# Kernel tuning notes

Hardware: AMD Instinct MI355X
Metric: run time of the kernel (lower is better)

Reference implementation:

```python
import jax, jax.numpy as jnp
import numpy as np

N_NODES = 100000


def _sage_conv(x, src, dst, w_l, b_l, w_r):
    # PyG SAGEConv (aggr='mean', root_weight=True):
    #   out = lin_l(mean_{j in N(i)} x_j) + lin_r(x_i)
    # messages flow src (row 0) -> dst (row 1)
    msgs = x[src]                                             # [E, d]
    agg = jax.ops.segment_sum(msgs, dst, num_segments=N_NODES)  # [N, d]
    cnt = jax.ops.segment_sum(jnp.ones((src.shape[0], 1), x.dtype), dst,
                              num_segments=N_NODES)           # [N, 1]
    mean = agg / jnp.maximum(cnt, 1.0)
    return mean @ w_l + b_l + x @ w_r


def setup_inputs() -> dict:
    key = jax.random.key(0)
    ks = jax.random.split(key, 8)
    in_dim, hid, out = 128, 64, 128
    n_edges = 1600000
    x = jax.random.normal(ks[0], (N_NODES, in_dim), dtype=jnp.float32)
    edge_index = jax.random.randint(ks[1], (2, n_edges), 0, N_NODES, dtype=jnp.int64)
    s1 = 1.0 / np.sqrt(in_dim)
    s2 = 1.0 / np.sqrt(hid)
    return {
        "x": x,
        "edge_index": edge_index,
        "w1_l": jax.random.uniform(ks[2], (in_dim, hid), jnp.float32, -s1, s1),
        "b1": jnp.zeros((hid,), jnp.float32),
        "w1_r": jax.random.uniform(ks[3], (in_dim, hid), jnp.float32, -s1, s1),
        "w2_l": jax.random.uniform(ks[4], (hid, out), jnp.float32, -s2, s2),
        "b2": jnp.zeros((out,), jnp.float32),
        "w2_r": jax.random.uniform(ks[5], (hid, out), jnp.float32, -s2, s2),
    }


def reference(x, edge_index, w1_l, b1, w1_r, w2_l, b2, w2_r):
    src, dst = edge_index[0], edge_index[1]
    h = jax.nn.relu(_sage_conv(x, src, dst, w1_l, b1, w1_r))
    h = _sage_conv(h, src, dst, w2_l, b2, w2_r)
    return h
```

## Files before the change

### kernel.cpp

```cpp
#include <hip/hip_runtime.h>

#define N_NODES 100000
#define NBUCK   782
#define P1TILE  8192
#define MAXB    4096

typedef __bf16 bf16x8 __attribute__((ext_vector_type(8)));
typedef float floatx4 __attribute__((ext_vector_type(4)));
typedef float floatx2 __attribute__((ext_vector_type(2)));

static __device__ __forceinline__ unsigned short f2bf(float f) {
  unsigned u = __float_as_uint(f);
  u += 0x7fff + ((u >> 16) & 1);
  return (unsigned short)(u >> 16);
}

__global__ __launch_bounds__(256) void bucket_count_kernel(
    const int* __restrict__ dst, int* __restrict__ bucket_cnt, int n_edges) {
  __shared__ int hist[NBUCK];
  for (int b = threadIdx.x; b < NBUCK; b += 256) hist[b] = 0;
  __syncthreads();
  int stride = gridDim.x * 256;
  for (int e = blockIdx.x * 256 + threadIdx.x; e < n_edges; e += stride)
    atomicAdd(&hist[dst[e] >> 7], 1);
  __syncthreads();
  for (int b = threadIdx.x; b < NBUCK; b += 256) {
    int c = hist[b];
    if (c) atomicAdd(&bucket_cnt[b], c);
  }
}

__global__ __launch_bounds__(256) void bucket_scan_kernel(
    const int* __restrict__ bucket_cnt, int* __restrict__ bucket_base,
    int* __restrict__ bucket_cursor) {
  __shared__ int tmp[256];
  int t = threadIdx.x;
  int loc[4];
  int s = 0;
  #pragma unroll
  for (int j = 0; j < 4; ++j) {
    int idx = 4 * t + j;
    loc[j] = s;
    s += (idx < NBUCK) ? bucket_cnt[idx] : 0;
  }
  tmp[t] = s;
  __syncthreads();
  for (int off = 1; off < 256; off <<= 1) {
    int u = (t >= off) ? tmp[t - off] : 0;
    __syncthreads();
    tmp[t] += u;
    __syncthreads();
  }
  int excl = tmp[t] - s;
  #pragma unroll
  for (int j = 0; j < 4; ++j) {
    int idx = 4 * t + j;
    if (idx < NBUCK) {
      int v = excl + loc[j];
      bucket_base[idx] = v;
      bucket_cursor[idx] = v;
    }
  }
  if (t == 255) bucket_base[NBUCK] = tmp[255];
}

__global__ __launch_bounds__(256) void bucket_partition_kernel(
    const int* __restrict__ src, const int* __restrict__ dst,
    int* __restrict__ bucket_cursor, unsigned* __restrict__ pairs,
    int n_edges) {
  __shared__ int hist[NBUCK];
  __shared__ int scan_[NBUCK];
  __shared__ int gbase[NBUCK];
  __shared__ int tmp[256];
  __shared__ int2 sorted[P1TILE];
  int t = threadIdx.x;
  long e0 = (long)blockIdx.x * P1TILE;
  int n = (int)min((long)P1TILE, (long)n_edges - e0);

  for (int b = t; b < NBUCK; b += 256) hist[b] = 0;
  __syncthreads();
  for (int i = t; i < n; i += 256) atomicAdd(&hist[dst[e0 + i] >> 7], 1);
  __syncthreads();

  int loc[4];
  int s = 0;
  #pragma unroll
  for (int j = 0; j < 4; ++j) {
    int idx = 4 * t + j;
    loc[j] = s;
    s += (idx < NBUCK) ? hist[idx] : 0;
  }
  tmp[t] = s;
  __syncthreads();
  for (int off = 1; off < 256; off <<= 1) {
    int u = (t >= off) ? tmp[t - off] : 0;
    __syncthreads();
    tmp[t] += u;
    __syncthreads();
  }
  int excl = tmp[t] - s;
  #pragma unroll
  for (int j = 0; j < 4; ++j) {
    int idx = 4 * t + j;
    if (idx < NBUCK) scan_[idx] = excl + loc[j];
  }
  __syncthreads();

  for (int b = t; b < NBUCK; b += 256) {
    int c = hist[b];
    gbase[b] = c ? atomicAdd(&bucket_cursor[b], c) : 0;
    hist[b] = scan_[b];
  }
  __syncthreads();

  for (int i = t; i < n; i += 256) {
    int sv = src[e0 + i];
    int dv = dst[e0 + i];
    int r = atomicAdd(&hist[dv >> 7], 1);
    sorted[r] = make_int2(sv, dv);
  }
  __syncthreads();

  for (int i = t; i < n; i += 256) {
    int2 p = sorted[i];
    int b = p.y >> 7;
    unsigned pk = (unsigned)p.x | ((unsigned)(p.y & 127) << 17);
    pairs[gbase[b] + (i - scan_[b])] = pk;
  }
}

__global__ __launch_bounds__(256) void bucket_csr_kernel(
    const unsigned* __restrict__ pairs, const int* __restrict__ bucket_base,
    int* __restrict__ offsets, int* __restrict__ src_sorted,
    int n_nodes, int n_edges) {
  __shared__ unsigned sp[MAXB];
  __shared__ int lout[MAXB];
  __shared__ int ndeg[128];
  __shared__ int nsc[128];
  int b = blockIdx.x;
  int node0 = b << 7;
  int t = threadIdx.x;
  int ebeg = bucket_base[b];
  int eend = bucket_base[b + 1];
  int m = eend - ebeg;
  bool fits = (m <= MAXB);
  if (t < 128) ndeg[t] = 0;
  __syncthreads();

  if (fits) {
    for (int i = t; i < m; i += 256) {
      unsigned p = pairs[ebeg + i];
      sp[i] = p;
      atomicAdd(&ndeg[p >> 17], 1);
    }
  } else {
    for (int i = t; i < m; i += 256)
      atomicAdd(&ndeg[pairs[ebeg + i] >> 17], 1);
  }
  __syncthreads();

  if (t < 128) nsc[t] = ndeg[t];
  __syncthreads();
  for (int off = 1; off < 128; off <<= 1) {
    int u = 0;
    if (t < 128 && t >= off) u = nsc[t - off];
    __syncthreads();
    if (t < 128) nsc[t] += u;
    __syncthreads();
  }
  if (t < 128) {
    int excl = nsc[t] - ndeg[t];
    int node = node0 + t;
    if (node < n_nodes) offsets[node] = ebeg + excl;
    ndeg[t] = excl;
  }
  if (b == NBUCK - 1 && t == 0) offsets[n_nodes] = n_edges;
  __syncthreads();

  if (fits) {
    for (int i = t; i < m; i += 256) {
      unsigned p = sp[i];
      int r = atomicAdd(&ndeg[p >> 17], 1);
      lout[r] = (int)(p & 0x1FFFFu);
    }
    __syncthreads();
    for (int i = t; i < m; i += 256) src_sorted[ebeg + i] = lout[i];
  } else {
    for (int i = t; i < m; i += 256) {
      unsigned p = pairs[ebeg + i];
      int r = atomicAdd(&ndeg[p >> 17], 1);
      src_sorted[ebeg + r] = (int)(p & 0x1FFFFu);
    }
  }
}

__global__ __launch_bounds__(128) void prep_weights_kernel(
    const float* __restrict__ w1_l, const float* __restrict__ w1_r,
    const float* __restrict__ w2_l, const float* __restrict__ w2_r,
    unsigned short* __restrict__ Wt1, unsigned short* __restrict__ Wt2) {
  int n = blockIdx.x, k = threadIdx.x;
  float v1 = (n < 64) ? w1_l[k * 64 + n] : w1_r[k * 64 + (n - 64)];
  Wt1[n * 128 + k] = f2bf(v1);
  float v2 = (k < 64) ? w2_l[k * 128 + n] : w2_r[(k - 64) * 128 + n];
  Wt2[n * 128 + k] = f2bf(v2);
}

template <int BIAS_MODE, bool OUT_BF16, bool A_F32>
__global__ __launch_bounds__(256) void mfma_gemm_kernel(
    const void* __restrict__ Av, const unsigned short* __restrict__ Wt,
    const float* __restrict__ bias, void* __restrict__ Y, int M) {
  __shared__ unsigned short As[64 * 136];
  int node0 = blockIdx.x * 64;
  int t = threadIdx.x;
  if (A_F32) {
    const float* A = (const float*)Av;
    #pragma unroll
    for (int i = 0; i < 8; ++i) {
      int c = t + i * 256;
      int row = c >> 5, c4 = (c & 31) * 4;
      float4 v = make_float4(0.f, 0.f, 0.f, 0.f);
      if (node0 + row < M) v = *(const float4*)&A[(long)(node0 + row) * 128 + c4];
      ushort4 o;
      o.x = f2bf(v.x); o.y = f2bf(v.y); o.z = f2bf(v.z); o.w = f2bf(v.w);
      *(ushort4*)&As[row * 136 + c4] = o;
    }
  } else {
    const unsigned short* A = (const unsigned short*)Av;
    #pragma unroll
    for (int i = 0; i < 4; ++i) {
      int c = t + i * 256;
      int row = c >> 4, c8 = (c & 15) * 8;
      uint4 v = make_uint4(0u, 0u, 0u, 0u);
      if (node0 + row < M) v = *(const uint4*)&A[(long)(node0 + row) * 128 + c8];
      *(uint4*)&As[row * 136 + c8] = v;
    }
  }
  __syncthreads();
  int w = t >> 6, lane = t & 63;
  int m = lane & 15, q = lane >> 4;
  int col0 = w * 32;
  floatx4 acc[4][2];
  #pragma unroll
  for (int rt = 0; rt < 4; ++rt)
    #pragma unroll
    for (int ct = 0; ct < 2; ++ct) acc[rt][ct] = (floatx4){0.f, 0.f, 0.f, 0.f};

  #pragma unroll
  for (int ks = 0; ks < 4; ++ks) {
    bf16x8 b0 = *(const bf16x8*)&Wt[(col0 + m) * 128 + ks * 32 + q * 8];
    bf16x8 b1 = *(const bf16x8*)&Wt[(col0 + 16 + m) * 128 + ks * 32 + q * 8];
    #pragma unroll
    for (int rt = 0; rt < 4; ++rt) {
      bf16x8 a = *(const bf16x8*)&As[(rt * 16 + m) * 136 + ks * 32 + q * 8];
      acc[rt][0] = __builtin_amdgcn_mfma_f32_16x16x32_bf16(a, b0, acc[rt][0], 0, 0, 0);
      acc[rt][1] = __builtin_amdgcn_mfma_f32_16x16x32_bf16(a, b1, acc[rt][1], 0, 0, 0);
    }
  }
  #pragma unroll
  for (int ct = 0; ct < 2; ++ct) {
    int col = col0 + ct * 16 + m;
    float bv = 0.f;
    if (BIAS_MODE == 1) bv = (col >= 64) ? bias[col - 64] : 0.f;
    if (BIAS_MODE == 2) bv = bias[col];
    #pragma unroll
    for (int rt = 0; rt < 4; ++rt) {
      #pragma unroll
      for (int i = 0; i < 4; ++i) {
        int row = node0 + rt * 16 + q * 4 + i;
        if (row >= M) continue;
        float v = acc[rt][ct][i] + bv;
        if (OUT_BF16) ((unsigned short*)Y)[(long)row * 128 + col] = f2bf(v);
        else          ((float*)Y)[(long)row * 128 + col] = v;
      }
    }
  }
}

#define ACC_V(v)                                                               \
  do {                                                                         \
    a01 += (floatx2){__uint_as_float((v).x << 16),                             \
                     __uint_as_float((v).x & 0xffff0000u)};                    \
    a23 += (floatx2){__uint_as_float((v).y << 16),                             \
                     __uint_as_float((v).y & 0xffff0000u)};                    \
    a45 += (floatx2){__uint_as_float((v).z << 16),                             \
                     __uint_as_float((v).z & 0xffff0000u)};                    \
    a67 += (floatx2){__uint_as_float((v).w << 16),                             \
                     __uint_as_float((v).w & 0xffff0000u)};                    \
  } while (0)

template <bool FUSE_RELU>
__global__ __launch_bounds__(256) void aggregate_bf16_kernel(
    const unsigned short* __restrict__ gsrc, const unsigned short* __restrict__ zadd,
    unsigned short* __restrict__ outp, const int* __restrict__ offsets,
    const int* __restrict__ src_sorted, int n_nodes) {
  int wid = (blockIdx.x * 256 + threadIdx.x) >> 6;
  int lane = threadIdx.x & 63;
  int node8 = wid << 3;
  if (node8 >= n_nodes) return;
  int sub = lane >> 3;
  int sl  = lane & 7;
  int node = node8 + sub;
  bool nvalid = (node < n_nodes);
  int beg = nvalid ? offsets[node] : 0;
  int end = nvalid ? offsets[node + 1] : 0;
  int deg = end - beg;

  int R = deg;
  R = max(R, __shfl_xor(R, 8, 64));
  R = max(R, __shfl_xor(R, 16, 64));
  R = max(R, __shfl_xor(R, 32, 64));

  const unsigned short* base = gsrc + sl * 8;
  floatx2 a01 = {0.f, 0.f}, a23 = {0.f, 0.f}, a45 = {0.f, 0.f}, a67 = {0.f, 0.f};

  int sidx = (sl < deg) ? src_sorted[beg + sl] : 0;
  int srcl = (lane & 56);

  for (int b = 0; b * 8 < R; ++b) {
    int sidx_nxt = 0;
    int nb = (b + 1) * 8;
    if (nb < R) {
      int p = nb + sl;
      if (p < deg) sidx_nxt = src_sorted[beg + p];
    }
    int k0 = b * 8;
    #pragma unroll
    for (int j = 0; j < 8; ++j) {
      int s = __shfl(sidx, srcl | j, 64);
      if (k0 + j < deg) {
        uint4 v = *(const uint4*)(base + (long)s * 128);
        ACC_V(v);
      }
    }
    sidx = sidx_nxt;
  }

  if (nvalid) {
    float inv = 1.f / fmaxf((float)deg, 1.f);
    float r[8];
    r[0] = a01.x * inv; r[1] = a01.y * inv;
    r[2] = a23.x * inv; r[3] = a23.y * inv;
    r[4] = a45.x * inv; r[5] = a45.y * inv;
    r[6] = a67.x * inv; r[7] = a67.y * inv;
    if (FUSE_RELU) {
      uint4 z = *(const uint4*)&zadd[(long)node * 128 + sl * 8];
      r[0] = fmaxf(r[0] + __uint_as_float(z.x << 16), 0.f);
      r[1] = fmaxf(r[1] + __uint_as_float(z.x & 0xffff0000u), 0.f);
      r[2] = fmaxf(r[2] + __uint_as_float(z.y << 16), 0.f);
      r[3] = fmaxf(r[3] + __uint_as_float(z.y & 0xffff0000u), 0.f);
      r[4] = fmaxf(r[4] + __uint_as_float(z.z << 16), 0.f);
      r[5] = fmaxf(r[5] + __uint_as_float(z.z & 0xffff0000u), 0.f);
      r[6] = fmaxf(r[6] + __uint_as_float(z.w << 16), 0.f);
      r[7] = fmaxf(r[7] + __uint_as_float(z.w & 0xffff0000u), 0.f);
    }
    uint4 ov;
    ov.x = (unsigned)f2bf(r[0]) | ((unsigned)f2bf(r[1]) << 16);
    ov.y = (unsigned)f2bf(r[2]) | ((unsigned)f2bf(r[3]) << 16);
    ov.z = (unsigned)f2bf(r[4]) | ((unsigned)f2bf(r[5]) << 16);
    ov.w = (unsigned)f2bf(r[6]) | ((unsigned)f2bf(r[7]) << 16);
    *(uint4*)&outp[(long)node * 128 + sl * 8] = ov;
  }
}
#undef ACC_V

extern "C" void kernel_launch(void* const* d_in, const int* in_sizes, int n_in,
                              void* d_out, int out_size, void* d_ws, size_t ws_size,
                              hipStream_t stream) {
  const float* x    = (const float*)d_in[0];
  const int*   ei   = (const int*)d_in[1];
  const float* w1_l = (const float*)d_in[2];
  const float* b1   = (const float*)d_in[3];
  const float* w1_r = (const float*)d_in[4];
  const float* w2_l = (const float*)d_in[5];
  const float* b2   = (const float*)d_in[6];
  const float* w2_r = (const float*)d_in[7];
  float* out = (float*)d_out;

  const int E = in_sizes[1] / 2;
  const int* src = ei;
  const int* dst = ei + E;

  unsigned short* ZB1 = (unsigned short*)d_ws;
  unsigned short* ZB2 = ZB1 + (long)N_NODES * 128;
  unsigned short* Wt1 = ZB2 + (long)N_NODES * 128;
  unsigned short* Wt2 = Wt1 + 16384;
  int* bucket_cnt    = (int*)(Wt2 + 16384);
  int* bucket_base   = bucket_cnt + NBUCK;
  int* bucket_cursor = bucket_base + NBUCK + 2;
  int* offsets       = bucket_cursor + NBUCK + 2;
  int* src_sorted    = offsets + N_NODES + 2;
  unsigned* pairs    = (unsigned*)(src_sorted + E);

  hipMemsetAsync(bucket_cnt, 0, (size_t)NBUCK * sizeof(int), stream);
  bucket_count_kernel<<<512, 256, 0, stream>>>(dst, bucket_cnt, E);
  bucket_scan_kernel<<<1, 256, 0, stream>>>(bucket_cnt, bucket_base,
                                            bucket_cursor);
  bucket_partition_kernel<<<(E + P1TILE - 1) / P1TILE, 256, 0, stream>>>(
      src, dst, bucket_cursor, pairs, E);
  bucket_csr_kernel<<<NBUCK, 256, 0, stream>>>(pairs, bucket_base, offsets,
                                               src_sorted, N_NODES, E);

  prep_weights_kernel<<<128, 128, 0, stream>>>(w1_l, w1_r, w2_l, w2_r, Wt1, Wt2);

  int gemm_blocks = (N_NODES + 63) / 64;
  int agg_blocks = (N_NODES + 31) / 32;

  mfma_gemm_kernel<1, true, true><<<gemm_blocks, 256, 0, stream>>>(
      x, Wt1, b1, ZB1, N_NODES);
  aggregate_bf16_kernel<true><<<agg_blocks, 256, 0, stream>>>(
      ZB1, ZB1 + 64, ZB2 + 64, offsets, src_sorted, N_NODES);

  aggregate_bf16_kernel<false><<<agg_blocks, 256, 0, stream>>>(
      ZB2 + 64, nullptr, ZB2, offsets, src_sorted, N_NODES);
  mfma_gemm_kernel<2, false, false><<<gemm_blocks, 256, 0, stream>>>(
      ZB2, Wt2, b2, out, N_NODES);
}
```

Before: 275.3 us.

## Stage per-wave edge source indices in LDS and unroll gather with independent accumulators

The aggregation kernel now loads each wave's contiguous range of sorted source indices into shared memory with coalesced loads, replacing the per-node register prefetch and shuffle broadcast. Each 8-lane group then walks its node's neighbours, issuing four row gathers per iteration into four independent accumulator sets to expose more memory-level parallelism. A fallback loop handles waves whose edge count exceeds the staging capacity. This adds a block-wide barrier, shared-memory usage, and more accumulator registers, which may reduce occupancy.

After: 267.1 us. -3.0%, faster.

```diff
diff --git a/kernel.cpp b/kernel.cpp
--- a/kernel.cpp
+++ b/kernel.cpp
@@ -4,6 +4,7 @@
 #define NBUCK   782
 #define P1TILE  8192
 #define MAXB    4096
+#define AGG_CAP 512
 
 typedef __bf16 bf16x8 __attribute__((ext_vector_type(8)));
 typedef float floatx4 __attribute__((ext_vector_type(4)));
@@ -276,16 +277,16 @@
   }
 }
 
-#define ACC_V(v)                                                               \
+#define ACC_P(A, v)                                                            \
   do {                                                                         \
-    a01 += (floatx2){__uint_as_float((v).x << 16),                             \
-                     __uint_as_float((v).x & 0xffff0000u)};                    \
-    a23 += (floatx2){__uint_as_float((v).y << 16),                             \
-                     __uint_as_float((v).y & 0xffff0000u)};                    \
-    a45 += (floatx2){__uint_as_float((v).z << 16),                             \
-                     __uint_as_float((v).z & 0xffff0000u)};                    \
-    a67 += (floatx2){__uint_as_float((v).w << 16),                             \
-                     __uint_as_float((v).w & 0xffff0000u)};                    \
+    A[0] += (floatx2){__uint_as_float((v).x << 16),                            \
+                      __uint_as_float((v).x & 0xffff0000u)};                   \
+    A[1] += (floatx2){__uint_as_float((v).y << 16),                            \
+                      __uint_as_float((v).y & 0xffff0000u)};                   \
+    A[2] += (floatx2){__uint_as_float((v).z << 16),                            \
+                      __uint_as_float((v).z & 0xffff0000u)};                   \
+    A[3] += (floatx2){__uint_as_float((v).w << 16),                            \
+                      __uint_as_float((v).w & 0xffff0000u)};                   \
   } while (0)
 
 template <bool FUSE_RELU>
@@ -293,55 +294,79 @@
     const unsigned short* __restrict__ gsrc, const unsigned short* __restrict__ zadd,
     unsigned short* __restrict__ outp, const int* __restrict__ offsets,
     const int* __restrict__ src_sorted, int n_nodes) {
-  int wid = (blockIdx.x * 256 + threadIdx.x) >> 6;
+  __shared__ int stage[4 * AGG_CAP];
+  int wv = threadIdx.x >> 6;
   int lane = threadIdx.x & 63;
+  int wid = (blockIdx.x << 2) | wv;
   int node8 = wid << 3;
-  if (node8 >= n_nodes) return;
   int sub = lane >> 3;
   int sl  = lane & 7;
   int node = node8 + sub;
-  bool nvalid = (node < n_nodes);
-  int beg = nvalid ? offsets[node] : 0;
-  int end = nvalid ? offsets[node + 1] : 0;
+  bool wvalid = (node8 < n_nodes);
+  bool nvalid = wvalid && (node < n_nodes);
+
+  int wbeg = 0, wend = 0, beg = 0, end = 0;
+  if (wvalid) {
+    wbeg = offsets[node8];
+    wend = offsets[min(node8 + 8, n_nodes)];
+  }
+  if (nvalid) {
+    beg = offsets[node];
+    end = offsets[node + 1];
+  }
   int deg = end - beg;
-
-  int R = deg;
-  R = max(R, __shfl_xor(R, 8, 64));
-  R = max(R, __shfl_xor(R, 16, 64));
-  R = max(R, __shfl_xor(R, 32, 64));
+  int cnt = wend - wbeg;
+  int* my = &stage[wv * AGG_CAP];
+  bool staged = wvalid && (cnt <= AGG_CAP);
+  if (staged) {
+    for (int i = lane; i < cnt; i += 64) my[i] = src_sorted[wbeg + i];
+  }
+  __syncthreads();
 
   const unsigned short* base = gsrc + sl * 8;
-  floatx2 a01 = {0.f, 0.f}, a23 = {0.f, 0.f}, a45 = {0.f, 0.f}, a67 = {0.f, 0.f};
-
-  int sidx = (sl < deg) ? src_sorted[beg + sl] : 0;
-  int srcl = (lane & 56);
-
-  for (int b = 0; b * 8 < R; ++b) {
-    int sidx_nxt = 0;
-    int nb = (b + 1) * 8;
-    if (nb < R) {
-      int p = nb + sl;
-      if (p < deg) sidx_nxt = src_sorted[beg + p];
-    }
-    int k0 = b * 8;
-    #pragma unroll
-    for (int j = 0; j < 8; ++j) {
-      int s = __shfl(sidx, srcl | j, 64);
-      if (k0 + j < deg) {
-        uint4 v = *(const uint4*)(base + (long)s * 128);
-        ACC_V(v);
-      }
-    }
-    sidx = sidx_nxt;
-  }
+  floatx2 A0[4], A1[4], A2[4], A3[4];
+  #pragma unroll
+  for (int i = 0; i < 4; ++i) {
+    A0[i] = (floatx2){0.f, 0.f}; A1[i] = (floatx2){0.f, 0.f};
+    A2[i] = (floatx2){0.f, 0.f}; A3[i] = (floatx2){0.f, 0.f};
+  }
+
+  if (staged) {
+    int lb = beg - wbeg;
+    int e = 0;
+    for (; e + 4 <= deg; e += 4) {
+      int s0 = my[lb + e];
+      int s1 = my[lb + e + 1];
+      int s2 = my[lb + e + 2];
+      int s3 = my[lb + e + 3];
+      uint4 v0 = *(const uint4*)(base + (long)s0 * 128);
+      uint4 v1 = *(const uint4*)(base + (long)s1 * 128);
+      uint4 v2 = *(const uint4*)(base + (long)s2 * 128);
+      uint4 v3 = *(const uint4*)(base + (long)s3 * 128);
+      ACC_P(A0, v0); ACC_P(A1, v1); ACC_P(A2, v2); ACC_P(A3, v3);
+    }
+    for (; e < deg; ++e) {
+      int s0 = my[lb + e];
+      uint4 v0 = *(const uint4*)(base + (long)s0 * 128);
+      ACC_P(A0, v0);
+    }
+  } else if (nvalid) {
+    for (int e = beg; e < end; ++e) {
+      int s0 = src_sorted[e];
+      uint4 v0 = *(const uint4*)(base + (long)s0 * 128);
+      ACC_P(A0, v0);
+    }
+  }
+  #pragma unroll
+  for (int i = 0; i < 4; ++i) A0[i] = (A0[i] + A1[i]) + (A2[i] + A3[i]);
 
   if (nvalid) {
     float inv = 1.f / fmaxf((float)deg, 1.f);
     float r[8];
-    r[0] = a01.x * inv; r[1] = a01.y * inv;
-    r[2] = a23.x * inv; r[3] = a23.y * inv;
-    r[4] = a45.x * inv; r[5] = a45.y * inv;
-    r[6] = a67.x * inv; r[7] = a67.y * inv;
+    r[0] = A0[0].x * inv; r[1] = A0[0].y * inv;
+    r[2] = A0[1].x * inv; r[3] = A0[1].y * inv;
+    r[4] = A0[2].x * inv; r[5] = A0[2].y * inv;
+    r[6] = A0[3].x * inv; r[7] = A0[3].y * inv;
     if (FUSE_RELU) {
       uint4 z = *(const uint4*)&zadd[(long)node * 128 + sl * 8];
       r[0] = fmaxf(r[0] + __uint_as_float(z.x << 16), 0.f);
@@ -361,7 +386,7 @@
     *(uint4*)&outp[(long)node * 128 + sl * 8] = ov;
   }
 }
-#undef ACC_V
+#undef ACC_P
 
 extern "C" void kernel_launch(void* const* d_in, const int* in_sizes, int n_in,
                               void* d_out, int out_size, void* d_ws, size_t ws_size,
```
